# Performance work log

Hardware: AMD Instinct MI355X
Metric: run time of the kernel (lower is better)

Reference implementation:

```python
import jax, jax.numpy as jnp
import numpy as np

NUM_EXPERTS = 8
HIDDEN = 2048
INTER = 1408
TOKENS = 2048
TOP_K = 2


def setup_inputs() -> dict:
    key = jax.random.key(0)
    ks = jax.random.split(key, 6)
    s_h = 1.0 / np.sqrt(HIDDEN)
    s_i = 1.0 / np.sqrt(INTER)
    hidden_states = jax.random.normal(ks[0], (TOKENS, HIDDEN), dtype=jnp.float32)
    top_k_index = jax.random.randint(ks[1], (TOKENS, TOP_K), 0, NUM_EXPERTS)
    w = jax.random.uniform(ks[2], (TOKENS, TOP_K), dtype=jnp.float32)
    top_k_weights = w / jnp.sum(w, axis=-1, keepdims=True)
    # weights stored as [E, in, out] for einsum (torch Linear is [out, in])
    gate_w = jax.random.uniform(ks[3], (NUM_EXPERTS, HIDDEN, INTER), jnp.float32, -s_h, s_h)
    up_w = jax.random.uniform(ks[4], (NUM_EXPERTS, HIDDEN, INTER), jnp.float32, -s_h, s_h)
    down_w = jax.random.uniform(ks[5], (NUM_EXPERTS, INTER, HIDDEN), jnp.float32, -s_i, s_i)
    return {
        "hidden_states": hidden_states,
        "top_k_index": top_k_index,
        "top_k_weights": top_k_weights,
        "gate_w": gate_w,
        "up_w": up_w,
        "down_w": down_w,
    }


def reference(hidden_states, top_k_index, top_k_weights, gate_w, up_w, down_w):
    # combine weight per (expert, token): w_et = sum_k topk_w[t,k] * [idx[t,k]==e]
    one_hot = jax.nn.one_hot(top_k_index, NUM_EXPERTS, dtype=hidden_states.dtype)  # [T,K,E]
    combine = jnp.einsum("tk,tke->et", top_k_weights, one_hot)  # [E,T]
    # dense per-expert SwiGLU MLP over all tokens (mask-combine form of the
    # gather/scatter loop; identical math since combine weight is 0 for
    # non-routed (expert, token) pairs)
    g = jnp.einsum("th,ehi->eti", hidden_states, gate_w)  # [E,T,I]
    u = jnp.einsum("th,ehi->eti", hidden_states, up_w)
    y = jnp.einsum("eti,eih->eth", jax.nn.silu(g) * u, down_w)  # [E,T,H]
    out = jnp.einsum("et,eth->th", combine, y)  # [T,H]
    return out
```

## Files before the change

### kernel.cpp

```cpp
#include <hip/hip_runtime.h>
#include <cstdint>
#include <cstddef>

#define NE 8
#define HD 2048
#define IN 1408
#define NT 2048
#define NP (NT*2)
#define MAXMT 40

typedef __bf16 bf16;
typedef __bf16 bf16x8 __attribute__((ext_vector_type(8)));
typedef __bf16 bf16x4 __attribute__((ext_vector_type(4)));
typedef float f32x4 __attribute__((ext_vector_type(4)));

__device__ __forceinline__ void load_lds16(const void* g, void* l) {
  __builtin_amdgcn_global_load_lds((const __attribute__((address_space(1))) uint32_t*)g,
                                   (__attribute__((address_space(3))) uint32_t*)l, 16, 0, 0);
}

__global__ void k_cvt(const float* __restrict__ x, bf16* __restrict__ y) {
  int i = blockIdx.x * 256 + threadIdx.x;
  f32x4 v = ((const f32x4*)x)[i];
  bf16x4 o;
  o[0] = (bf16)v[0]; o[1] = (bf16)v[1]; o[2] = (bf16)v[2]; o[3] = (bf16)v[3];
  ((bf16x4*)y)[i] = o;
}

__global__ void k_route(const int* __restrict__ idx, const float* __restrict__ w,
                        int* __restrict__ perm_tok, float* __restrict__ perm_w,
                        int* __restrict__ slot_of, int* __restrict__ tiles,
                        int* __restrict__ bmap1, int* __restrict__ bmap2) {
  __shared__ int cnt[NE], off[NE + 1], rk[NE], sb[NE + 1];
  int tid = threadIdx.x;
  if (tid < NE) { cnt[tid] = 0; rk[tid] = 0; }
  __syncthreads();
  for (int a = tid; a < NP; a += 256) atomicAdd(&cnt[idx[a]], 1);
  __syncthreads();
  if (tid == 0) { off[0] = 0; for (int e = 0; e < NE; e++) off[e + 1] = off[e] + cnt[e]; }
  __syncthreads();
  for (int a = tid; a < NP; a += 256) {
    int e = idx[a];
    int p = off[e] + atomicAdd(&rk[e], 1);
    perm_tok[p] = a >> 1;
    perm_w[p] = w[a];
    slot_of[a] = p;
  }
  __syncthreads();
  if (tid == 0) {
    int n = 0;
    for (int e = 0; e < NE; e++)
      for (int r = off[e]; r < off[e + 1]; r += 128) {
        tiles[n] = e; tiles[MAXMT + n] = r; tiles[2 * MAXMT + n] = off[e + 1];
        n++;
      }
    for (int s = n; s < MAXMT; s++) tiles[s] = -1;
    tiles[3 * MAXMT] = n;
    int a = 0;
    for (int e = 0; e < NE; e++) { sb[e] = a; a += (cnt[e] + 127) >> 7; }
    sb[NE] = a;
  }
  __syncthreads();
  if (tid < NE) {
    int e = tid, s0 = sb[e], s1 = sb[e + 1];
    int j1 = s0 * 11, j2 = s0 * 16;
    for (int nt = 0; nt < 11; nt++)
      for (int s = s0; s < s1; s++) bmap1[j1++] = s | (nt << 16);
    for (int nt = 0; nt < 16; nt++)
      for (int s = s0; s < s1; s++) bmap2[j2++] = s | (nt << 16);
  }
}

#define MM_COMPUTE(kk) do { \
    const bf16* Ab_ = As + ((kk) & 1) * (128 * 64); \
    const bf16* Bb_ = Bs + ((kk) & 1) * (128 * 64); \
    _Pragma("unroll") \
    for (int ks = 0; ks < 2; ks++) { \
      int ckf = ks * 4 + (lane >> 4); \
      bf16x8 af[4], bfr[4]; \
      _Pragma("unroll") \
      for (int fm = 0; fm < 4; fm++) { \
        int m_ = wm + fm * 16 + (lane & 15); \
        af[fm] = *(const bf16x8*)(Ab_ + (m_ * 8 + (ckf ^ (m_ & 7))) * 8); \
      } \
      _Pragma("unroll") \
      for (int fn = 0; fn < 4; fn++) { \
        int n_ = wn + fn * 16 + (lane & 15); \
        bfr[fn] = *(const bf16x8*)(Bb_ + (n_ * 8 + (ckf ^ (n_ & 7))) * 8); \
      } \
      __builtin_amdgcn_s_setprio(1); \
      _Pragma("unroll") \
      for (int fm = 0; fm < 4; fm++) \
        _Pragma("unroll") \
        for (int fn = 0; fn < 4; fn++) \
          acc[fm][fn] = __builtin_amdgcn_mfma_f32_16x16x32_bf16(af[fm], bfr[fn], acc[fm][fn], 0, 0, 0); \
      __builtin_amdgcn_s_setprio(0); \
    } \
  } while (0)

#define MM_BODY(kk, vCon, vLoad, WSTR) do { \
    { int k0a = ((kk) + 1) * 64; \
      bf16* dA_ = As + (((kk) + 1) & 1) * (128 * 64); \
      _Pragma("unroll") \
      for (int i2 = 0; i2 < 4; i2++) load_lds16(aG[i2] + k0a, dA_ + aOff[i2]); } \
    __builtin_amdgcn_sched_barrier(0); \
    if ((kk) + 2 < NK) { int k0b = ((kk) + 2) * 64; \
      _Pragma("unroll") \
      for (int j = 0; j < 8; j++) vLoad[j] = *(const f32x4*)(gB + (size_t)(k0b + j) * NTOT); } \
    MM_COMPUTE(kk); \
    { bf16* Bw_ = Bs + (((kk) + 1) & 1) * (128 * 64); \
      _Pragma("unroll") \
      for (int i2 = 0; i2 < 4; i2++) { bf16x8 o; \
        _Pragma("unroll") for (int j = 0; j < 8; j++) o[j] = (bf16)vCon[j][i2]; \
        *(bf16x8*)(Bw_ + bslot[i2]) = o; } } \
    asm volatile("s_waitcnt " WSTR ::: "memory"); \
    __builtin_amdgcn_s_barrier(); \
    __builtin_amdgcn_sched_barrier(0); \
  } while (0)

template<int KTOT, int NTOT, bool GATHER>
__device__ __forceinline__ void mm_pipe(const bf16* __restrict__ A,
                                        const float* __restrict__ Bsrc,
                                        const int* __restrict__ perm_tok,
                                        int row0, int rowend, int nb,
                                        float* __restrict__ C) {
  constexpr int NK = KTOT / 64;
  __shared__ __align__(16) bf16 As[2 * 128 * 64];
  __shared__ __align__(16) bf16 Bs[2 * 128 * 64];

  int tid = threadIdx.x;
  int lane = tid & 63, wave = tid >> 6;
  int wm = (wave >> 1) * 64, wn = (wave & 1) * 64;

  const bf16* aG[4]; int aOff[4];
#pragma unroll
  for (int i2 = 0; i2 < 4; i2++) {
    int s = i2 * 256 + tid;
    int r = s >> 3, c = (s & 7) ^ (r & 7);
    int tr = row0 + r; if (tr > NP - 1) tr = NP - 1;
    int arow = GATHER ? perm_tok[tr] : tr;
    aG[i2] = A + (size_t)arow * KTOT + c * 8;
    aOff[i2] = s * 8;
  }
  int kk0 = (tid & 7) * 8, nn = (tid >> 3) * 4;
  const float* gB = Bsrc + (size_t)kk0 * NTOT + (nb + nn);
  int bslot[4];
#pragma unroll
  for (int i2 = 0; i2 < 4; i2++) { int n = nn + i2; bslot[i2] = (n * 8 + ((tid & 7) ^ (n & 7))) * 8; }

  f32x4 acc[4][4] = {};
  f32x4 vA[8], vB[8];

#pragma unroll
  for (int i2 = 0; i2 < 4; i2++) load_lds16(aG[i2], As + aOff[i2]);
  __builtin_amdgcn_sched_barrier(0);
#pragma unroll
  for (int j = 0; j < 8; j++) vA[j] = *(const f32x4*)(gB + (size_t)j * NTOT);
#pragma unroll
  for (int j = 0; j < 8; j++) vB[j] = *(const f32x4*)(gB + (size_t)(64 + j) * NTOT);
#pragma unroll
  for (int i2 = 0; i2 < 4; i2++) {
    bf16x8 o;
#pragma unroll
    for (int j = 0; j < 8; j++) o[j] = (bf16)vA[j][i2];
    *(bf16x8*)(Bs + bslot[i2]) = o;
  }
  asm volatile("s_waitcnt vmcnt(8) lgkmcnt(0)" ::: "memory");
  __builtin_amdgcn_s_barrier();
  __builtin_amdgcn_sched_barrier(0);

#pragma unroll 1
  for (int k = 0; k + 2 < NK; k += 2) {
    MM_BODY(k,     vB, vA, "vmcnt(8) lgkmcnt(0)");
    MM_BODY(k + 1, vA, vB, "vmcnt(8) lgkmcnt(0)");
  }
  MM_BODY(NK - 2, vB, vA, "vmcnt(0) lgkmcnt(0)");
  MM_COMPUTE(NK - 1);

#pragma unroll
  for (int fm = 0; fm < 4; fm++) {
#pragma unroll
    for (int rr = 0; rr < 4; rr++) {
      int m = wm + fm * 16 + ((lane >> 4) << 2) + rr;
      int row = row0 + m;
      if (row < rowend) {
#pragma unroll
        for (int fn = 0; fn < 4; fn++) {
          int n = nb + wn + fn * 16 + (lane & 15);
          C[(size_t)row * NTOT + n] = acc[fm][fn][rr];
        }
      }
    }
  }
}

__device__ __forceinline__ int xcd_logical(int b, int W) {
  int xcd = b & 7, p = b >> 3;
  int q = W >> 3, r = W & 7;
  int cs = xcd < r ? q + 1 : q;
  if (p >= cs) return -1;
  return (xcd < r ? xcd * (q + 1) : r * (q + 1) + (xcd - r) * q) + p;
}

__launch_bounds__(256, 2)
__global__ void k_mm1(const bf16* __restrict__ hid, const float* __restrict__ gw,
                      const float* __restrict__ uw, const int* __restrict__ perm_tok,
                      const int* __restrict__ tiles, const int* __restrict__ bmap1,
                      float* __restrict__ g, float* __restrict__ u) {
  int nsl = tiles[3 * MAXMT];
  int hn = 11 * nsl;
  int l = xcd_logical(blockIdx.x, 2 * hn);
  if (l < 0) return;
  int half = l >= hn ? 1 : 0;
  int m = bmap1[l - half * hn];
  int slot = m & 0xffff, nt = m >> 16;
  int e = tiles[slot];
  int row0 = tiles[MAXMT + slot], rowend = tiles[2 * MAXMT + slot];
  const float* B = (half ? uw : gw) + (size_t)e * HD * IN;
  float* C = half ? u : g;
  mm_pipe<HD, IN, true>(hid, B, perm_tok, row0, rowend, nt * 128, C);
}

__global__ void k_act(const float* __restrict__ g, const float* __restrict__ u,
                      const float* __restrict__ pw, bf16* __restrict__ act) {
  int i = blockIdx.x * 256 + threadIdx.x;
  int row = i / (IN / 8);
  float w = pw[row];
  f32x4 g0 = ((const f32x4*)g)[2 * i], g1 = ((const f32x4*)g)[2 * i + 1];
  f32x4 u0 = ((const f32x4*)u)[2 * i], u1 = ((const f32x4*)u)[2 * i + 1];
  bf16x8 o;
#pragma unroll
  for (int j = 0; j < 4; j++) {
    float s = g0[j] / (1.0f + __expf(-g0[j]));
    o[j] = (bf16)(s * u0[j] * w);
  }
#pragma unroll
  for (int j = 0; j < 4; j++) {
    float s = g1[j] / (1.0f + __expf(-g1[j]));
    o[4 + j] = (bf16)(s * u1[j] * w);
  }
  ((bf16x8*)act)[i] = o;
}

__launch_bounds__(256, 2)
__global__ void k_mm2(const bf16* __restrict__ act, const float* __restrict__ dw,
                      const int* __restrict__ tiles, const int* __restrict__ bmap2,
                      float* __restrict__ pout) {
  int nsl = tiles[3 * MAXMT];
  int l = xcd_logical(blockIdx.x, 16 * nsl);
  if (l < 0) return;
  int m = bmap2[l];
  int slot = m & 0xffff, nt = m >> 16;
  int e = tiles[slot];
  int row0 = tiles[MAXMT + slot], rowend = tiles[2 * MAXMT + slot];
  mm_pipe<IN, HD, false>(act, dw + (size_t)e * IN * HD, nullptr, row0, rowend, nt * 128, pout);
}

__global__ void k_comb(const float* __restrict__ pout, const int* __restrict__ slot_of,
                       float* __restrict__ out) {
  int i = blockIdx.x * 256 + threadIdx.x;
  int t = i >> 9;
  int hc = i & 511;
  f32x4 a = ((const f32x4*)(pout + (size_t)slot_of[2 * t] * HD))[hc];
  f32x4 c = ((const f32x4*)(pout + (size_t)slot_of[2 * t + 1] * HD))[hc];
  ((f32x4*)(out + (size_t)t * HD))[hc] = a + c;
}

extern "C" void kernel_launch(void* const* d_in, const int* in_sizes, int n_in,
                              void* d_out, int out_size, void* d_ws, size_t ws_size,
                              hipStream_t stream) {
  const float* hidden  = (const float*)d_in[0];
  const int*   tk_idx  = (const int*)d_in[1];
  const float* tk_w    = (const float*)d_in[2];
  const float* gw      = (const float*)d_in[3];
  const float* uw      = (const float*)d_in[4];
  const float* dw      = (const float*)d_in[5];
  float* out = (float*)d_out;

  char* ws = (char*)d_ws;
  int*   perm_tok = (int*)ws;
  float* perm_w   = (float*)(ws + 16384);
  int*   slot_of  = (int*)(ws + 32768);
  int*   tiles    = (int*)(ws + 49152);
  int*   bmap1    = (int*)(ws + 50176);
  int*   bmap2    = (int*)(ws + 52224);
  bf16*  hid_bf   = (bf16*)(ws + 65536);
  bf16*  act      = (bf16*)(ws + 65536 + 8388608);
  char*  xbase    = ws + 65536 + 8388608 + 11534336;
  float* gbuf     = (float*)xbase;
  float* ubuf     = (float*)(xbase + 23068672);
  float* pout     = (float*)xbase;

  k_cvt  <<<4096, 256, 0, stream>>>(hidden, hid_bf);
  k_route<<<1,    256, 0, stream>>>(tk_idx, tk_w, perm_tok, perm_w, slot_of, tiles, bmap1, bmap2);
  k_mm1  <<<880,  256, 0, stream>>>(hid_bf, gw, uw, perm_tok, tiles, bmap1, gbuf, ubuf);
  k_act  <<<2816, 256, 0, stream>>>(gbuf, ubuf, perm_w, act);
  k_mm2  <<<640,  256, 0, stream>>>(act, dw, tiles, bmap2, pout);
  k_comb <<<4096, 256, 0, stream>>>(pout, slot_of, out);
}
```

Measured before the change: 479.9 us.

## Pre-convert and transpose expert weights to bf16, simplify GEMM to direct LDS loads

Adds a kernel that converts each fp32 expert weight matrix into a transposed bf16 copy in workspace before the GEMMs. Both GEMMs can then fetch B with the same global-to-LDS DMA path as A, so the in-loop fp32 register loads and conversion go away. The hand-pipelined double-buffered main loop is replaced by a simple single-buffered loop with two __syncthreads per k-step, which gives up load/compute overlap. The extra conversion pass reads all weights once more and writes a bf16 copy, and a fallback reuses one buffer with split launches when the workspace is small.

```diff
diff --git a/kernel.cpp b/kernel.cpp
--- a/kernel.cpp
+++ b/kernel.cpp
@@ -25,6 +25,33 @@
   bf16x4 o;
   o[0] = (bf16)v[0]; o[1] = (bf16)v[1]; o[2] = (bf16)v[2]; o[3] = (bf16)v[3];
   ((bf16x4*)y)[i] = o;
+}
+
+template<int K, int N>
+__global__ void k_cvtw(const float* __restrict__ src, bf16* __restrict__ dst) {
+  constexpr int KT = K / 128, NT2 = N / 64;
+  int b = blockIdx.x;
+  int e = b / (KT * NT2), rem = b % (KT * NT2);
+  int kt = rem / NT2, ntl = rem % NT2;
+  const float* S = src + (size_t)e * K * N + (size_t)kt * 128 * N + ntl * 64;
+  bf16* D = dst + (size_t)e * N * K + (size_t)ntl * 64 * K + kt * 128;
+  __shared__ __align__(16) float T[128 * 68];
+  int tid = threadIdx.x;
+#pragma unroll
+  for (int p = 0; p < 8; p++) {
+    int r = p * 16 + (tid >> 4), c4 = (tid & 15) * 4;
+    *(f32x4*)(T + r * 68 + c4) = *(const f32x4*)(S + (size_t)r * N + c4);
+  }
+  __syncthreads();
+  int n = tid >> 2;
+#pragma unroll
+  for (int p = 0; p < 4; p++) {
+    int k0 = (p * 4 + (tid & 3)) * 8;
+    bf16x8 o;
+#pragma unroll
+    for (int j = 0; j < 8; j++) o[j] = (bf16)T[(k0 + j) * 68 + n];
+    *(bf16x8*)(D + (size_t)n * K + k0) = o;
+  }
 }
 
 __global__ void k_route(const int* __restrict__ idx, const float* __restrict__ w,
@@ -71,68 +98,20 @@
   }
 }
 
-#define MM_COMPUTE(kk) do { \
-    const bf16* Ab_ = As + ((kk) & 1) * (128 * 64); \
-    const bf16* Bb_ = Bs + ((kk) & 1) * (128 * 64); \
-    _Pragma("unroll") \
-    for (int ks = 0; ks < 2; ks++) { \
-      int ckf = ks * 4 + (lane >> 4); \
-      bf16x8 af[4], bfr[4]; \
-      _Pragma("unroll") \
-      for (int fm = 0; fm < 4; fm++) { \
-        int m_ = wm + fm * 16 + (lane & 15); \
-        af[fm] = *(const bf16x8*)(Ab_ + (m_ * 8 + (ckf ^ (m_ & 7))) * 8); \
-      } \
-      _Pragma("unroll") \
-      for (int fn = 0; fn < 4; fn++) { \
-        int n_ = wn + fn * 16 + (lane & 15); \
-        bfr[fn] = *(const bf16x8*)(Bb_ + (n_ * 8 + (ckf ^ (n_ & 7))) * 8); \
-      } \
-      __builtin_amdgcn_s_setprio(1); \
-      _Pragma("unroll") \
-      for (int fm = 0; fm < 4; fm++) \
-        _Pragma("unroll") \
-        for (int fn = 0; fn < 4; fn++) \
-          acc[fm][fn] = __builtin_amdgcn_mfma_f32_16x16x32_bf16(af[fm], bfr[fn], acc[fm][fn], 0, 0, 0); \
-      __builtin_amdgcn_s_setprio(0); \
-    } \
-  } while (0)
-
-#define MM_BODY(kk, vCon, vLoad, WSTR) do { \
-    { int k0a = ((kk) + 1) * 64; \
-      bf16* dA_ = As + (((kk) + 1) & 1) * (128 * 64); \
-      _Pragma("unroll") \
-      for (int i2 = 0; i2 < 4; i2++) load_lds16(aG[i2] + k0a, dA_ + aOff[i2]); } \
-    __builtin_amdgcn_sched_barrier(0); \
-    if ((kk) + 2 < NK) { int k0b = ((kk) + 2) * 64; \
-      _Pragma("unroll") \
-      for (int j = 0; j < 8; j++) vLoad[j] = *(const f32x4*)(gB + (size_t)(k0b + j) * NTOT); } \
-    MM_COMPUTE(kk); \
-    { bf16* Bw_ = Bs + (((kk) + 1) & 1) * (128 * 64); \
-      _Pragma("unroll") \
-      for (int i2 = 0; i2 < 4; i2++) { bf16x8 o; \
-        _Pragma("unroll") for (int j = 0; j < 8; j++) o[j] = (bf16)vCon[j][i2]; \
-        *(bf16x8*)(Bw_ + bslot[i2]) = o; } } \
-    asm volatile("s_waitcnt " WSTR ::: "memory"); \
-    __builtin_amdgcn_s_barrier(); \
-    __builtin_amdgcn_sched_barrier(0); \
-  } while (0)
-
 template<int KTOT, int NTOT, bool GATHER>
-__device__ __forceinline__ void mm_pipe(const bf16* __restrict__ A,
-                                        const float* __restrict__ Bsrc,
+__device__ __forceinline__ void mm_core(const bf16* __restrict__ A,
+                                        const bf16* __restrict__ WT,
                                         const int* __restrict__ perm_tok,
                                         int row0, int rowend, int nb,
                                         float* __restrict__ C) {
-  constexpr int NK = KTOT / 64;
-  __shared__ __align__(16) bf16 As[2 * 128 * 64];
-  __shared__ __align__(16) bf16 Bs[2 * 128 * 64];
+  __shared__ __align__(16) bf16 As[128 * 64];
+  __shared__ __align__(16) bf16 Bs[128 * 64];
 
   int tid = threadIdx.x;
   int lane = tid & 63, wave = tid >> 6;
   int wm = (wave >> 1) * 64, wn = (wave & 1) * 64;
 
-  const bf16* aG[4]; int aOff[4];
+  const bf16* aG[4]; const bf16* bG[4]; int sOff[4];
 #pragma unroll
   for (int i2 = 0; i2 < 4; i2++) {
     int s = i2 * 256 + tid;
@@ -140,42 +119,40 @@
     int tr = row0 + r; if (tr > NP - 1) tr = NP - 1;
     int arow = GATHER ? perm_tok[tr] : tr;
     aG[i2] = A + (size_t)arow * KTOT + c * 8;
-    aOff[i2] = s * 8;
-  }
-  int kk0 = (tid & 7) * 8, nn = (tid >> 3) * 4;
-  const float* gB = Bsrc + (size_t)kk0 * NTOT + (nb + nn);
-  int bslot[4];
-#pragma unroll
-  for (int i2 = 0; i2 < 4; i2++) { int n = nn + i2; bslot[i2] = (n * 8 + ((tid & 7) ^ (n & 7))) * 8; }
+    bG[i2] = WT + (size_t)(nb + r) * KTOT + c * 8;
+    sOff[i2] = s * 8;
+  }
 
   f32x4 acc[4][4] = {};
-  f32x4 vA[8], vB[8];
-
-#pragma unroll
-  for (int i2 = 0; i2 < 4; i2++) load_lds16(aG[i2], As + aOff[i2]);
-  __builtin_amdgcn_sched_barrier(0);
-#pragma unroll
-  for (int j = 0; j < 8; j++) vA[j] = *(const f32x4*)(gB + (size_t)j * NTOT);
-#pragma unroll
-  for (int j = 0; j < 8; j++) vB[j] = *(const f32x4*)(gB + (size_t)(64 + j) * NTOT);
-#pragma unroll
-  for (int i2 = 0; i2 < 4; i2++) {
-    bf16x8 o;
-#pragma unroll
-    for (int j = 0; j < 8; j++) o[j] = (bf16)vA[j][i2];
-    *(bf16x8*)(Bs + bslot[i2]) = o;
-  }
-  asm volatile("s_waitcnt vmcnt(8) lgkmcnt(0)" ::: "memory");
-  __builtin_amdgcn_s_barrier();
-  __builtin_amdgcn_sched_barrier(0);
-
-#pragma unroll 1
-  for (int k = 0; k + 2 < NK; k += 2) {
-    MM_BODY(k,     vB, vA, "vmcnt(8) lgkmcnt(0)");
-    MM_BODY(k + 1, vA, vB, "vmcnt(8) lgkmcnt(0)");
-  }
-  MM_BODY(NK - 2, vB, vA, "vmcnt(0) lgkmcnt(0)");
-  MM_COMPUTE(NK - 1);
+
+  for (int k0 = 0; k0 < KTOT; k0 += 64) {
+    __syncthreads();
+#pragma unroll
+    for (int i2 = 0; i2 < 4; i2++) load_lds16(aG[i2] + k0, As + sOff[i2]);
+#pragma unroll
+    for (int i2 = 0; i2 < 4; i2++) load_lds16(bG[i2] + k0, Bs + sOff[i2]);
+    __syncthreads();
+#pragma unroll
+    for (int ks = 0; ks < 2; ks++) {
+      int ckf = ks * 4 + (lane >> 4);
+      bf16x8 af[4], bfr[4];
+#pragma unroll
+      for (int fm = 0; fm < 4; fm++) {
+        int m_ = wm + fm * 16 + (lane & 15);
+        af[fm] = *(const bf16x8*)(As + (m_ * 8 + (ckf ^ (m_ & 7))) * 8);
+      }
+#pragma unroll
+      for (int fn = 0; fn < 4; fn++) {
+        int n_ = wn + fn * 16 + (lane & 15);
+        bfr[fn] = *(const bf16x8*)(Bs + (n_ * 8 + (ckf ^ (n_ & 7))) * 8);
+      }
+#pragma unroll
+      for (int fm = 0; fm < 4; fm++)
+#pragma unroll
+        for (int fn = 0; fn < 4; fn++)
+          acc[fm][fn] = __builtin_amdgcn_mfma_f32_16x16x32_bf16(af[fm], bfr[fn], acc[fm][fn], 0, 0, 0);
+    }
+  }
 
 #pragma unroll
   for (int fm = 0; fm < 4; fm++) {
@@ -203,22 +180,23 @@
 }
 
 __launch_bounds__(256, 2)
-__global__ void k_mm1(const bf16* __restrict__ hid, const float* __restrict__ gw,
-                      const float* __restrict__ uw, const int* __restrict__ perm_tok,
+__global__ void k_mm1(const bf16* __restrict__ hid, const bf16* __restrict__ gwt,
+                      const bf16* __restrict__ uwt, const int* __restrict__ perm_tok,
                       const int* __restrict__ tiles, const int* __restrict__ bmap1,
-                      float* __restrict__ g, float* __restrict__ u) {
+                      float* __restrict__ g, float* __restrict__ u, int halfsel) {
   int nsl = tiles[3 * MAXMT];
   int hn = 11 * nsl;
-  int l = xcd_logical(blockIdx.x, 2 * hn);
+  int W = (halfsel < 0) ? 2 * hn : hn;
+  int l = xcd_logical(blockIdx.x, W);
   if (l < 0) return;
-  int half = l >= hn ? 1 : 0;
-  int m = bmap1[l - half * hn];
+  int half = (halfsel < 0) ? (l >= hn ? 1 : 0) : halfsel;
+  int li = (halfsel < 0) ? (l - (l >= hn ? hn : 0)) : l;
+  int m = bmap1[li];
   int slot = m & 0xffff, nt = m >> 16;
   int e = tiles[slot];
   int row0 = tiles[MAXMT + slot], rowend = tiles[2 * MAXMT + slot];
-  const float* B = (half ? uw : gw) + (size_t)e * HD * IN;
-  float* C = half ? u : g;
-  mm_pipe<HD, IN, true>(hid, B, perm_tok, row0, rowend, nt * 128, C);
+  const bf16* WTp = (half ? uwt : gwt) + (size_t)e * IN * HD;
+  mm_core<HD, IN, true>(hid, WTp, perm_tok, row0, rowend, nt * 128, half ? u : g);
 }
 
 __global__ void k_act(const float* __restrict__ g, const float* __restrict__ u,
@@ -243,7 +221,7 @@
 }
 
 __launch_bounds__(256, 2)
-__global__ void k_mm2(const bf16* __restrict__ act, const float* __restrict__ dw,
+__global__ void k_mm2(const bf16* __restrict__ act, const bf16* __restrict__ dwt,
                       const int* __restrict__ tiles, const int* __restrict__ bmap2,
                       float* __restrict__ pout) {
   int nsl = tiles[3 * MAXMT];
@@ -253,7 +231,7 @@
   int slot = m & 0xffff, nt = m >> 16;
   int e = tiles[slot];
   int row0 = tiles[MAXMT + slot], rowend = tiles[2 * MAXMT + slot];
-  mm_pipe<IN, HD, false>(act, dw + (size_t)e * IN * HD, nullptr, row0, rowend, nt * 128, pout);
+  mm_core<IN, HD, false>(act, dwt + (size_t)e * HD * IN, nullptr, row0, rowend, nt * 128, pout);
 }
 
 __global__ void k_comb(const float* __restrict__ pout, const int* __restrict__ slot_of,
@@ -284,17 +262,50 @@
   int*   tiles    = (int*)(ws + 49152);
   int*   bmap1    = (int*)(ws + 50176);
   int*   bmap2    = (int*)(ws + 52224);
-  bf16*  hid_bf   = (bf16*)(ws + 65536);
-  bf16*  act      = (bf16*)(ws + 65536 + 8388608);
-  char*  xbase    = ws + 65536 + 8388608 + 11534336;
-  float* gbuf     = (float*)xbase;
-  float* ubuf     = (float*)(xbase + 23068672);
-  float* pout     = (float*)xbase;
+
+  const size_t base   = 65536;
+  const size_t sz_hid = 8388608;
+  const size_t sz_act = 11534336;
+  const size_t sz_wt  = 46137344;
+  const size_t sz_g   = 23068672;
+
+  bf16* hid_bf = (bf16*)(ws + base);
+  bf16* act    = (bf16*)(ws + base + sz_hid);
+  char* wbase  = ws + base + sz_hid + sz_act;
+
+  bool wide = ws_size >= base + sz_hid + sz_act + 3 * sz_wt + 2 * sz_g;
 
   k_cvt  <<<4096, 256, 0, stream>>>(hidden, hid_bf);
   k_route<<<1,    256, 0, stream>>>(tk_idx, tk_w, perm_tok, perm_w, slot_of, tiles, bmap1, bmap2);
-  k_mm1  <<<880,  256, 0, stream>>>(hid_bf, gw, uw, perm_tok, tiles, bmap1, gbuf, ubuf);
-  k_act  <<<2816, 256, 0, stream>>>(gbuf, ubuf, perm_w, act);
-  k_mm2  <<<640,  256, 0, stream>>>(act, dw, tiles, bmap2, pout);
-  k_comb <<<4096, 256, 0, stream>>>(pout, slot_of, out);
-}
+
+  if (wide) {
+    bf16* gwt = (bf16*)wbase;
+    bf16* uwt = (bf16*)(wbase + sz_wt);
+    bf16* dwt = (bf16*)(wbase + 2 * sz_wt);
+    float* g  = (float*)(wbase + 3 * sz_wt);
+    float* u  = (float*)(wbase + 3 * sz_wt + sz_g);
+    float* pout = (float*)wbase;
+
+    k_cvtw<HD, IN><<<2816, 256, 0, stream>>>(gw, gwt);
+    k_cvtw<HD, IN><<<2816, 256, 0, stream>>>(uw, uwt);
+    k_cvtw<IN, HD><<<2816, 256, 0, stream>>>(dw, dwt);
+    k_mm1 <<<880,  256, 0, stream>>>(hid_bf, gwt, uwt, perm_tok, tiles, bmap1, g, u, -1);
+    k_act <<<2816, 256, 0, stream>>>(g, u, perm_w, act);
+    k_mm2 <<<640,  256, 0, stream>>>(act, dwt, tiles, bmap2, pout);
+    k_comb<<<4096, 256, 0, stream>>>(pout, slot_of, out);
+  } else {
+    bf16* wt  = (bf16*)wbase;
+    float* g  = (float*)(wbase + sz_wt);
+    float* u  = (float*)(wbase + sz_wt + sz_g);
+    float* pout = (float*)(wbase + sz_wt);
+
+    k_cvtw<HD, IN><<<2816, 256, 0, stream>>>(gw, wt);
+    k_mm1 <<<448,  256, 0, stream>>>(hid_bf, wt, wt, perm_tok, tiles, bmap1, g, u, 0);
+    k_cvtw<HD, IN><<<2816, 256, 0, stream>>>(uw, wt);
+    k_mm1 <<<448,  256, 0, stream>>>(hid_bf, wt, wt, perm_tok, tiles, bmap1, g, u, 1);
+    k_act <<<2816, 256, 0, stream>>>(g, u, perm_w, act);
+    k_cvtw<IN, HD><<<2816, 256, 0, stream>>>(dw, wt);
+    k_mm2 <<<640,  256, 0, stream>>>(act, wt, tiles, bmap2, pout);
+    k_comb<<<4096, 256, 0, stream>>>(pout, slot_of, out);
+  }
+}
```

New measurement: 467.8 us. 2.5% less time.
